# Kernel tuning notes

Hardware: AMD Instinct MI355X
Metric: run time of the kernel (lower is better)

## Reference

```python
import jax, jax.numpy as jnp
import numpy as np

B, C, H, W = 8, 512, 64, 64
K = 19       # num classes (Cityscapes)
CT = 256     # transform channels


def _proj(x, w, g, b):
    # 1x1 conv (no bias) + folded eval-mode BatchNorm (per-channel scale g, bias b) + ReLU
    # x: [B,Cin,H,W], w: [Cout,Cin]
    y = jnp.einsum('bchw,oc->bohw', x, w)
    return jax.nn.relu(y * g[None, :, None, None] + b[None, :, None, None])


def setup_inputs() -> dict:
    key = jax.random.key(0)
    ks = jax.random.split(key, 12)
    s = lambda i, shape: jax.random.normal(ks[i], shape, jnp.float32) * 0.05
    ones = lambda n: jnp.ones((n,), jnp.float32)
    zeros = lambda n: jnp.zeros((n,), jnp.float32)
    return {
        'x': jax.random.normal(ks[0], (B, C, H, W), jnp.float32),
        'preds': jax.random.normal(ks[1], (B, K, H, W), jnp.float32),
        'feats_il': jax.random.normal(ks[2], (B, C, H, W), jnp.float32),
        # query_project: two 1x1 conv+BN+ReLU blocks
        'q_w1': s(3, (CT, C)), 'q_g1': ones(CT), 'q_b1': zeros(CT),
        'q_w2': s(4, (CT, CT)), 'q_g2': ones(CT), 'q_b2': zeros(CT),
        # key_project: two 1x1 conv+BN+ReLU blocks
        'k_w1': s(5, (CT, C)), 'k_g1': ones(CT), 'k_b1': zeros(CT),
        'k_w2': s(6, (CT, CT)), 'k_g2': ones(CT), 'k_b2': zeros(CT),
        # value_project: one 1x1 conv+BN+ReLU (value_out_norm=True)
        'v_w': s(7, (CT, C)), 'v_g': ones(CT), 'v_b': zeros(CT),
        # out_project: one 1x1 conv+BN+ReLU
        'o_w': s(8, (C, CT)), 'o_g': ones(C), 'o_b': zeros(C),
    }


def reference(x, preds, feats_il, q_w1, q_g1, q_b1, q_w2, q_g2, q_b2,
              k_w1, k_g1, k_b1, k_w2, k_g2, k_b2, v_w, v_g, v_b, o_w, o_g, o_b):
    b, c, h, w = x.shape
    k = preds.shape[1]
    hw = h * w
    feats = x.reshape(b, c, hw).transpose(0, 2, 1)        # [B,HW,C]
    logits = preds.reshape(b, k, hw).transpose(0, 2, 1)   # [B,HW,K]
    argmax = jnp.argmax(logits, axis=-1)                  # [B,HW]
    onehot = jax.nn.one_hot(argmax, k, dtype=x.dtype)     # [B,HW,K]
    NEG = jnp.asarray(-1e9, x.dtype)
    masked = jnp.where(onehot > 0, logits, NEG)
    # per-class softmax over the pixels assigned to that class
    wgt = jax.nn.softmax(masked, axis=1)                  # [B,HW,K]
    cls_feat = jnp.einsum('bpk,bpc->bkc', wgt, feats)     # [B,K,C]
    # scatter class descriptor back to every pixel of that class
    feats_sl = jnp.take_along_axis(cls_feat, argmax[:, :, None], axis=1)  # [B,HW,C]
    feats_sl = feats_sl.transpose(0, 2, 1).reshape(b, c, h, w)
    # SelfAttentionBlock: query from inputs, key/value from feats_sl
    q = _proj(_proj(x, q_w1, q_g1, q_b1), q_w2, q_g2, q_b2)
    kk = _proj(_proj(feats_sl, k_w1, k_g1, k_b1), k_w2, k_g2, k_b2)
    v = _proj(feats_sl, v_w, v_g, v_b)
    ct = q.shape[1]
    qf = q.reshape(b, ct, hw).transpose(0, 2, 1)          # [B,HW,CT]
    kf = kk.reshape(b, ct, hw)                            # [B,CT,HW]
    vf = v.reshape(b, ct, hw).transpose(0, 2, 1)          # [B,HW,CT]
    sim = jnp.einsum('bqc,bck->bqk', qf, kf) * (ct ** -0.5)
    attn = jax.nn.softmax(sim, axis=-1)
    ctx = jnp.einsum('bqk,bkc->bqc', attn, vf)            # [B,HW,CT]
    ctx = ctx.transpose(0, 2, 1).reshape(b, ct, h, w)
    return _proj(ctx, o_w, o_g, o_b)
```

## Files before the change

kernel.cpp:

```cpp
#include <hip/hip_runtime.h>
#include <math.h>

#define HW 4096
#define NB 8
#define NK 19
#define CIN 512
#define CTC 256

typedef __attribute__((ext_vector_type(8))) short short8;
typedef __attribute__((ext_vector_type(4))) float f32x4;

__device__ inline unsigned short f2bf(float x) {
  unsigned u = __float_as_uint(x);
  return (unsigned short)((u + 0x7fffu + ((u >> 16) & 1u)) >> 16);
}
__device__ inline float bf2f(unsigned short h) {
  return __uint_as_float(((unsigned)h) << 16);
}
__device__ inline void gload16(const void* g, void* l) {
  __builtin_amdgcn_global_load_lds(
      (const __attribute__((address_space(1))) void*)g,
      (__attribute__((address_space(3))) void*)l, 16, 0, 0);
}

__global__ __launch_bounds__(256) void wk1a(
    const float* __restrict__ w1, const float* __restrict__ w2,
    const float* __restrict__ wo, unsigned short* __restrict__ wb1,
    unsigned short* __restrict__ wb2, unsigned short* __restrict__ wbo,
    uint4* __restrict__ cls_feat_z, const float* __restrict__ preds,
    float* __restrict__ bestg, int* __restrict__ clsg,
    unsigned int* __restrict__ Mu_part, unsigned int* __restrict__ cnt_part) {
  __shared__ unsigned int Mw[NK];
  __shared__ unsigned int Cw[NK];
  int bx = blockIdx.x;
  int tid = threadIdx.x;
  if (bx < 320) {
    int gid = bx * 256 + tid;
    int i = gid * 4;
    const float* src;
    unsigned short* dst;
    int off;
    if (i < 131072) { src = w1; dst = wb1; off = i; }
    else if (i < 196608) { src = w2; dst = wb2; off = i - 131072; }
    else { src = wo; dst = wbo; off = i - 196608; }
    float4 v = *(const float4*)(src + off);
    dst[off + 0] = f2bf(v.x);
    dst[off + 1] = f2bf(v.y);
    dst[off + 2] = f2bf(v.z);
    dst[off + 3] = f2bf(v.w);
    uint4 z = {0u, 0u, 0u, 0u};
    for (int j = gid; j < 19456; j += 81920) cls_feat_z[j] = z;
  } else {
    int bq = bx - 320;
    int b = bq >> 4, pblk = bq & 15;
    if (tid < NK) { Mw[tid] = 0u; Cw[tid] = 0u; }
    __syncthreads();
    int p = pblk * 256 + tid;
    const float* pb = preds + (size_t)b * NK * HW;
    float best = pb[p];
    int bi = 0;
#pragma unroll
    for (int k = 1; k < NK; ++k) {
      float v = pb[k * HW + p];
      if (v > best) { best = v; bi = k; }
    }
    bestg[b * HW + p] = best;
    clsg[b * HW + p] = bi;
    unsigned fb = __float_as_uint(best);
    unsigned key = (fb & 0x80000000u) ? ~fb : (fb | 0x80000000u);
    atomicMax(&Mw[bi], key);
    atomicAdd(&Cw[bi], 1u);
    __syncthreads();
    if (tid < 32) {
      Mu_part[(b * 16 + pblk) * 32 + tid] = (tid < NK) ? Mw[tid] : 0u;
      cnt_part[(b * 16 + pblk) * 32 + tid] = (tid < NK) ? Cw[tid] : 0u;
    }
  }
}

__global__ __launch_bounds__(256) void k1b(
    float* __restrict__ bestg, const int* __restrict__ clsg,
    const unsigned int* __restrict__ Mu_part, float* __restrict__ Zf_part) {
  int b = blockIdx.y, pblk = blockIdx.x;
  int tid = threadIdx.x;
  __shared__ float Mf[NK];
  __shared__ float Zw[NK];
  if (tid < NK) {
    unsigned key = 0u;
#pragma unroll
    for (int j = 0; j < 16; ++j) {
      unsigned v = Mu_part[(b * 16 + j) * 32 + tid];
      key = (v > key) ? v : key;
    }
    float m = -1e30f;
    if (key) {
      unsigned fb = (key & 0x80000000u) ? (key & 0x7fffffffu) : ~key;
      m = __uint_as_float(fb);
    }
    Mf[tid] = m;
    Zw[tid] = 0.f;
  }
  __syncthreads();
  int p = pblk * 256 + tid;
  int c = clsg[b * HW + p];
  float e = expf(bestg[b * HW + p] - Mf[c]);
  bestg[b * HW + p] = e;
  atomicAdd(&Zw[c], e);
  __syncthreads();
  if (tid < 32) Zf_part[(b * 16 + pblk) * 32 + tid] = (tid < NK) ? Zw[tid] : 0.f;
}

__global__ __launch_bounds__(256) void xk2(
    const float* __restrict__ x, const float* __restrict__ eg,
    const int* __restrict__ clsg, const float* __restrict__ Zf_part,
    unsigned short* __restrict__ xT, float* __restrict__ cls_feat) {
  __shared__ float tile[64][65];
  __shared__ unsigned short Bs[32 * 516];
  __shared__ float Zl[NK];
  int b = blockIdx.z, c0 = blockIdx.y * 64, pbase = blockIdx.x * 512;
  int tid = threadIdx.x;
  int l = tid & 63, w = tid >> 6;
  if (tid < NK) {
    float s = 0.f;
#pragma unroll
    for (int j = 0; j < 16; ++j) s += Zf_part[(b * 16 + j) * 32 + tid];
    Zl[tid] = s;
  }
  {
    uint4 z = {0u, 0u, 0u, 0u};
    for (int i = tid; i < 2064; i += 256) ((uint4*)Bs)[i] = z;
  }
  __syncthreads();
  for (int i = tid; i < 512; i += 256) {
    int c = clsg[b * HW + pbase + i];
    Bs[c * 516 + i] = f2bf(eg[b * HW + pbase + i] / Zl[c]);
  }
  f32x4 acc[2];
  acc[0] = (f32x4){0.f, 0.f, 0.f, 0.f};
  acc[1] = (f32x4){0.f, 0.f, 0.f, 0.f};
  int cbase = w * 16;
  for (int s = 0; s < 8; ++s) {
    int ps = pbase + s * 64;
    __syncthreads();
#pragma unroll
    for (int r = 0; r < 4; ++r) {
      int cl = r * 16 + (tid >> 4);
      int pl = (tid & 15) * 4;
      float4 v = *(const float4*)&x[((size_t)b * CIN + c0 + cl) * HW + ps + pl];
      tile[cl][pl + 0] = v.x;
      tile[cl][pl + 1] = v.y;
      tile[cl][pl + 2] = v.z;
      tile[cl][pl + 3] = v.w;
    }
    __syncthreads();
#pragma unroll
    for (int j = 0; j < 16; ++j) {
      int ploc = j * 4 + w;
      xT[((size_t)b * HW + ps + ploc) * CIN + c0 + l] = f2bf(tile[l][ploc]);
    }
#pragma unroll
    for (int ch = 0; ch < 2; ++ch) {
      int pt = ch * 32 + (l >> 4) * 8;
      union { short8 v; unsigned short u[8]; } af;
      const float* tp = &tile[cbase + (l & 15)][pt];
#pragma unroll
      for (int j = 0; j < 8; ++j) af.u[j] = f2bf(tp[j]);
      int pg = s * 64 + pt;
#pragma unroll
      for (int mf = 0; mf < 2; ++mf) {
        short8 bf = *(const short8*)&Bs[(mf * 16 + (l & 15)) * 516 + pg];
        acc[mf] =
            __builtin_amdgcn_mfma_f32_16x16x32_bf16(af.v, bf, acc[mf], 0, 0, 0);
      }
    }
  }
#pragma unroll
  for (int mf = 0; mf < 2; ++mf) {
    int k = mf * 16 + (l & 15);
    if (k < NK) {
#pragma unroll
      for (int r = 0; r < 4; ++r) {
        int c = c0 + cbase + (l >> 4) * 4 + r;
        atomicAdd(&cls_feat[((size_t)b * NK + k) * CIN + c], acc[mf][r]);
      }
    }
  }
}

__global__ __launch_bounds__(256) void k3a(
    const float* __restrict__ cls_feat, const float* __restrict__ kw1,
    const float* __restrict__ kg1, const float* __restrict__ kb1,
    const float* __restrict__ vw, const float* __restrict__ vg,
    const float* __restrict__ vb, float* __restrict__ h1g,
    float* __restrict__ Vcls) {
  int bk = blockIdx.y;
  int b = bk / NK, kc = bk % NK;
  int q = blockIdx.x;
  __shared__ float cf[CIN];
  int tid = threadIdx.x;
  const float* row = cls_feat + (size_t)bk * CIN;
  for (int i = tid; i < CIN; i += 256) cf[i] = row[i];
  __syncthreads();
  int o = tid >> 1, half = tid & 1;
  int col = q * 64 + (o & 63);
  const float* w =
      (o < 64) ? &kw1[(size_t)col * CIN] : &vw[(size_t)col * CIN];
  int base = half * 256;
  float acc[4] = {0.f, 0.f, 0.f, 0.f};
#pragma unroll 8
  for (int i = 0; i < 64; ++i) {
    float4 w4 = *(const float4*)&w[base + i * 4];
    const float* c4 = &cf[base + i * 4];
    acc[i & 3] += w4.x * c4[0] + w4.y * c4[1] + w4.z * c4[2] + w4.w * c4[3];
  }
  float s = (acc[0] + acc[1]) + (acc[2] + acc[3]);
  s += __shfl_xor(s, 1);
  if (half == 0) {
    if (o < 64) {
      h1g[(size_t)bk * CTC + col] = fmaxf(s * kg1[col] + kb1[col], 0.f);
    } else {
      Vcls[((size_t)b * CTC + col) * NK + kc] =
          fmaxf(s * vg[col] + vb[col], 0.f);
    }
  }
}

__global__ __launch_bounds__(256) void k3b(
    const float* __restrict__ h1g, const float* __restrict__ kw2,
    const float* __restrict__ kg2, const float* __restrict__ kb2,
    unsigned short* __restrict__ KclsT) {
  int bk = blockIdx.y;
  int q = blockIdx.x;
  __shared__ float h1[CTC];
  int tid = threadIdx.x;
  const float* row = h1g + (size_t)bk * CTC;
  if (tid < CTC) h1[tid] = row[tid];
  __syncthreads();
  int o = tid >> 2, part = tid & 3;
  int col = q * 64 + o;
  const float* w = &kw2[(size_t)col * CTC + part * 64];
  const float* c = &h1[part * 64];
  float acc[4] = {0.f, 0.f, 0.f, 0.f};
#pragma unroll
  for (int i = 0; i < 16; ++i) {
    float4 w4 = *(const float4*)&w[i * 4];
    acc[i & 3] += w4.x * c[i * 4] + w4.y * c[i * 4 + 1] + w4.z * c[i * 4 + 2] +
                  w4.w * c[i * 4 + 3];
  }
  float s = (acc[0] + acc[1]) + (acc[2] + acc[3]);
  s += __shfl_xor(s, 1);
  s += __shfl_xor(s, 2);
  if (part == 0)
    KclsT[(size_t)bk * CTC + col] = f2bf(fmaxf(s * kg2[col] + kb2[col], 0.f));
}

template <int KD>
__global__ __launch_bounds__(256) void gemm_mfma(
    const unsigned short* __restrict__ A, const unsigned short* __restrict__ Wb,
    const float* __restrict__ g, const float* __restrict__ bb,
    void* __restrict__ Y, int M, int outmode) {
  __shared__ __align__(16) unsigned short As[2][128 * 32];
  __shared__ __align__(16) unsigned short Bs[2][128 * 32];
  int b = blockIdx.z;
  int n0 = blockIdx.x * 128;
  int m0 = blockIdx.y * 128;
  int tid = threadIdx.x;
  int l = tid & 63, wid = tid >> 6;
  int wr = wid >> 1, wc = wid & 1;
  const unsigned short* Ab = A + (size_t)b * HW * KD;

  f32x4 acc[4][4];
#pragma unroll
  for (int i = 0; i < 4; ++i)
#pragma unroll
    for (int j = 0; j < 4; ++j) acc[i][j] = (f32x4){0.f, 0.f, 0.f, 0.f};

  const int NT = KD / 32;
  auto STAGE = [&](int buf, int t) {
    int k0 = t * 32;
#pragma unroll
    for (int q = 0; q < 2; ++q) {
      int e = q * 2048 + tid * 8;
      int rl = e >> 5, sl = (e >> 3) & 3;
      gload16(Ab + (size_t)(n0 + rl) * KD + k0 + 8 * (sl ^ ((rl >> 1) & 3)),
              &As[buf][q * 2048 + wid * 512]);
    }
#pragma unroll
    for (int q = 0; q < 2; ++q) {
      int e = q * 2048 + tid * 8;
      int rl = e >> 5, sl = (e >> 3) & 3;
      gload16(Wb + (size_t)(m0 + rl) * KD + k0 + 8 * (sl ^ ((rl >> 1) & 3)),
              &Bs[buf][q * 2048 + wid * 512]);
    }
  };
  STAGE(0, 0);
  for (int t = 0; t < NT; ++t) {
    __syncthreads();
    if (t + 1 < NT) STAGE((t + 1) & 1, t + 1);
    int cur = t & 1;
    short8 af[4], bf[4];
#pragma unroll
    for (int f = 0; f < 4; ++f) {
      int nl = wr * 64 + f * 16 + (l & 15);
      af[f] = *(const short8*)&As[cur][nl * 32 + 8 * ((l >> 4) ^ ((nl >> 1) & 3))];
      int ml = wc * 64 + f * 16 + (l & 15);
      bf[f] = *(const short8*)&Bs[cur][ml * 32 + 8 * ((l >> 4) ^ ((ml >> 1) & 3))];
    }
#pragma unroll
    for (int i = 0; i < 4; ++i)
#pragma unroll
      for (int j = 0; j < 4; ++j)
        acc[i][j] =
            __builtin_amdgcn_mfma_f32_16x16x32_bf16(af[i], bf[j], acc[i][j], 0, 0, 0);
  }
  if (outmode == 0) {
    float* Yf = (float*)Y + (size_t)b * M * HW;
#pragma unroll
    for (int j = 0; j < 4; ++j) {
      int m = m0 + wc * 64 + j * 16 + (l & 15);
      float gm = g[m], bm = bb[m];
#pragma unroll
      for (int i = 0; i < 4; ++i) {
        int n = n0 + wr * 64 + i * 16 + (l >> 4) * 4;
        float4 o;
        o.x = fmaxf(acc[i][j][0] * gm + bm, 0.f);
        o.y = fmaxf(acc[i][j][1] * gm + bm, 0.f);
        o.z = fmaxf(acc[i][j][2] * gm + bm, 0.f);
        o.w = fmaxf(acc[i][j][3] * gm + bm, 0.f);
        *(float4*)&Yf[(size_t)m * HW + n] = o;
      }
    }
  } else {
    unsigned short* Yt = (unsigned short*)Y + (size_t)b * HW * M;
#pragma unroll
    for (int j = 0; j < 4; ++j) {
      int m = m0 + wc * 64 + j * 16 + (l & 15);
      float gm = g[m], bm = bb[m];
#pragma unroll
      for (int i = 0; i < 4; ++i) {
        int n = n0 + wr * 64 + i * 16 + (l >> 4) * 4;
#pragma unroll
        for (int r = 0; r < 4; ++r)
          Yt[(size_t)(n + r) * M + m] = f2bf(fmaxf(acc[i][j][r] * gm + bm, 0.f));
      }
    }
  }
}

__global__ __launch_bounds__(256, 1) void g2k5(
    const unsigned short* __restrict__ q1T, const unsigned short* __restrict__ W2,
    const float* __restrict__ g2, const float* __restrict__ b2,
    const unsigned short* __restrict__ KclsT, const float* __restrict__ Vcls,
    const unsigned int* __restrict__ cnt_part, unsigned short* __restrict__ ctxT) {
  __shared__ __align__(16) char RC[49152];
  __shared__ __align__(16) unsigned short Qf[8][4096];
  __shared__ __align__(16) unsigned short Kl2[32 * 32 * 8];
  __shared__ __align__(16) unsigned short Vl2[4 * 256 * 8];
  __shared__ float cntl[NK];
  unsigned short* As = (unsigned short*)RC;
  unsigned short* Bs = (unsigned short*)(RC + 16384);
  float* simT = (float*)RC;
  unsigned short* Pl = (unsigned short*)(RC + 16896);

  int b = blockIdx.y;
  int p0 = blockIdx.x * 128;
  int tid = threadIdx.x;
  int l = tid & 63, w = tid >> 6;
  const unsigned short* q1b = q1T + ((size_t)b * HW + p0) * CTC;

  for (int i = tid; i < NK * 32; i += 256) {
    int m = i >> 5, s = i & 31;
    short8 v = *(const short8*)&KclsT[((size_t)b * NK + m) * CTC + s * 8];
    *(short8*)&Kl2[(s * 32 + m) * 8] = v;
  }
  for (int i = tid; i < 4 * 256; i += 256) {
    int s = i >> 8, c = i & 255;
    union { short8 v; unsigned short u[8]; } pk;
    const float* vr = &Vcls[((size_t)b * CTC + c) * NK];
#pragma unroll
    for (int j = 0; j < 8; ++j) {
      int k = s * 8 + j;
      pk.u[j] = (k < NK) ? f2bf(vr[k]) : (unsigned short)0;
    }
    *(short8*)&Vl2[(s * 256 + c) * 8] = pk.v;
  }
  if (tid < NK) {
    unsigned int s = 0u;
#pragma unroll
    for (int j = 0; j < 16; ++j) s += cnt_part[(b * 16 + j) * 32 + tid];
    cntl[tid] = (float)s;
  }

  auto STAGE_A = [&](int buf, int t) {
    int k0 = t * 32;
#pragma unroll
    for (int q = 0; q < 2; ++q) {
      int e = q * 2048 + tid * 8;
      int rl = e >> 5, sl = (e >> 3) & 3;
      gload16(q1b + (size_t)rl * CTC + k0 + 8 * (sl ^ ((rl >> 1) & 3)),
              &As[buf * 4096 + q * 2048 + w * 512]);
    }
  };
  auto STAGE_B = [&](int buf, int t) {
    int k0 = t * 32;
#pragma unroll
    for (int q = 0; q < 4; ++q) {
      int e = q * 2048 + tid * 8;
      int rl = e >> 5, sl = (e >> 3) & 3;
      gload16(W2 + (size_t)rl * CTC + k0 + 8 * (sl ^ ((rl >> 1) & 3)),
              &Bs[buf * 8192 + q * 2048 + w * 512]);
    }
  };
  f32x4 acc[2][16];
#pragma unroll
  for (int i = 0; i < 2; ++i)
#pragma unroll
    for (int j = 0; j < 16; ++j) acc[i][j] = (f32x4){0.f, 0.f, 0.f, 0.f};
  STAGE_A(0, 0);
  STAGE_B(0, 0);
  for (int t = 0; t < 8; ++t) {
    __syncthreads();
    if (t + 1 < 8) { STAGE_A((t + 1) & 1, t + 1); STAGE_B((t + 1) & 1, t + 1); }
    int cur = t & 1;
    short8 af[2];
#pragma unroll
    for (int f = 0; f < 2; ++f) {
      int nl = w * 32 + f * 16 + (l & 15);
      af[f] =
          *(const short8*)&As[cur * 4096 + nl * 32 + 8 * ((l >> 4) ^ ((nl >> 1) & 3))];
    }
#pragma unroll
    for (int mf = 0; mf < 16; ++mf) {
      int ml = mf * 16 + (l & 15);
      short8 bf =
          *(const short8*)&Bs[cur * 8192 + ml * 32 + 8 * ((l >> 4) ^ ((ml >> 1) & 3))];
      acc[0][mf] =
          __builtin_amdgcn_mfma_f32_16x16x32_bf16(af[0], bf, acc[0][mf], 0, 0, 0);
      acc[1][mf] =
          __builtin_amdgcn_mfma_f32_16x16x32_bf16(af[1], bf, acc[1][mf], 0, 0, 0);
    }
  }
#pragma unroll
  for (int mf = 0; mf < 16; ++mf) {
    int ch = mf * 16 + (l & 15);
    float gm = g2[ch], bm = b2[ch];
    int tq = ch >> 5, slot = (ch >> 3) & 3, wi = ch & 7;
#pragma unroll
    for (int i = 0; i < 2; ++i) {
#pragma unroll
      for (int r = 0; r < 4; ++r) {
        int p = w * 32 + i * 16 + (l >> 4) * 4 + r;
        Qf[tq][p * 32 + 8 * (slot ^ ((p >> 1) & 3)) + wi] =
            f2bf(fmaxf(acc[i][mf][r] * gm + bm, 0.f));
      }
    }
  }
  __syncthreads();

  f32x4 a2[2][2];
#pragma unroll
  for (int i = 0; i < 2; ++i)
#pragma unroll
    for (int j = 0; j < 2; ++j) a2[i][j] = (f32x4){0.f, 0.f, 0.f, 0.f};
  for (int t = 0; t < 8; ++t) {
    short8 aq[2], bk[2];
#pragma unroll
    for (int f = 0; f < 2; ++f) {
      int nl = w * 32 + f * 16 + (l & 15);
      aq[f] = *(const short8*)&Qf[t][nl * 32 + 8 * ((l >> 4) ^ ((nl >> 1) & 3))];
      int s = t * 4 + (l >> 4);
      int ml = f * 16 + (l & 15);
      bk[f] = *(const short8*)&Kl2[(s * 32 + ml) * 8];
    }
#pragma unroll
    for (int i = 0; i < 2; ++i)
#pragma unroll
      for (int j = 0; j < 2; ++j)
        a2[i][j] =
            __builtin_amdgcn_mfma_f32_16x16x32_bf16(aq[i], bk[j], a2[i][j], 0, 0, 0);
  }
  __syncthreads();
#pragma unroll
  for (int i = 0; i < 2; ++i)
#pragma unroll
    for (int j = 0; j < 2; ++j) {
      int m = j * 16 + (l & 15);
      if (m < NK) {
#pragma unroll
        for (int r = 0; r < 4; ++r) {
          int p = w * 32 + i * 16 + (l >> 4) * 4 + r;
          simT[p * 33 + m] = a2[i][j][r];
        }
      }
    }
  __syncthreads();
  if (tid < 128) {
    float sims[NK];
#pragma unroll
    for (int k = 0; k < NK; ++k) sims[k] = simT[tid * 33 + k] * 0.0625f;
    float m = -1e30f;
#pragma unroll
    for (int k = 0; k < NK; ++k)
      if (cntl[k] > 0.f) m = fmaxf(m, sims[k]);
    float d = 0.f;
#pragma unroll
    for (int k = 0; k < NK; ++k) {
      float e = (cntl[k] > 0.f) ? expf(sims[k] - m) : 0.f;
      sims[k] = cntl[k] * e;
      d += sims[k];
    }
    float inv = 1.f / d;
#pragma unroll
    for (int s = 0; s < 4; ++s) {
      union { short8 v; unsigned short u8[8]; } pk;
#pragma unroll
      for (int j = 0; j < 8; ++j) {
        int k = s * 8 + j;
        pk.u8[j] = (k < NK) ? f2bf(sims[k] * inv) : (unsigned short)0;
      }
      *(short8*)&Pl[(s * 128 + tid) * 8] = pk.v;
    }
  }
  __syncthreads();
  short8 ap[2];
#pragma unroll
  for (int f = 0; f < 2; ++f) {
    int nl = w * 32 + f * 16 + (l & 15);
    ap[f] = *(const short8*)&Pl[((l >> 4) * 128 + nl) * 8];
  }
  unsigned short* cb = ctxT + ((size_t)b * HW + p0) * CTC;
#pragma unroll
  for (int mc = 0; mc < 4; ++mc) {
#pragma unroll
    for (int mf = 0; mf < 4; ++mf) {
      int ml = mc * 64 + mf * 16 + (l & 15);
      short8 bv = *(const short8*)&Vl2[((l >> 4) * 256 + ml) * 8];
#pragma unroll
      for (int nf = 0; nf < 2; ++nf) {
        f32x4 z = {0.f, 0.f, 0.f, 0.f};
        f32x4 o = __builtin_amdgcn_mfma_f32_16x16x32_bf16(ap[nf], bv, z, 0, 0, 0);
#pragma unroll
        for (int r = 0; r < 4; ++r) {
          int p = w * 32 + nf * 16 + (l >> 4) * 4 + r;
          cb[(size_t)p * CTC + ml] = f2bf(o[r]);
        }
      }
    }
  }
}

extern "C" void kernel_launch(void* const* d_in, const int* in_sizes, int n_in,
                              void* d_out, int out_size, void* d_ws, size_t ws_size,
                              hipStream_t stream) {
  const float* x = (const float*)d_in[0];
  const float* preds = (const float*)d_in[1];
  const float* q_w1 = (const float*)d_in[3];
  const float* q_g1 = (const float*)d_in[4];
  const float* q_b1 = (const float*)d_in[5];
  const float* q_w2 = (const float*)d_in[6];
  const float* q_g2 = (const float*)d_in[7];
  const float* q_b2 = (const float*)d_in[8];
  const float* k_w1 = (const float*)d_in[9];
  const float* k_g1 = (const float*)d_in[10];
  const float* k_b1 = (const float*)d_in[11];
  const float* k_w2 = (const float*)d_in[12];
  const float* k_g2 = (const float*)d_in[13];
  const float* k_b2 = (const float*)d_in[14];
  const float* v_w = (const float*)d_in[15];
  const float* v_g = (const float*)d_in[16];
  const float* v_b = (const float*)d_in[17];
  const float* o_w = (const float*)d_in[18];
  const float* o_g = (const float*)d_in[19];
  const float* o_b = (const float*)d_in[20];
  float* out = (float*)d_out;

  char* base = (char*)d_ws;
  unsigned short* xT = (unsigned short*)base;
  unsigned short* q1T = (unsigned short*)(base + 33554432);
  unsigned short* ctxT = q1T;
  char* f32r = base + 50331648;
  float* cls_feat = (float*)f32r;
  unsigned short* KclsT = (unsigned short*)(f32r + 311296);
  float* Vcls = (float*)(f32r + 389120);
  unsigned short* wb1 = (unsigned short*)(f32r + 544768);
  unsigned short* wb2 = (unsigned short*)(f32r + 806912);
  unsigned short* wbo = (unsigned short*)(f32r + 937984);
  float* h1g = (float*)(f32r + 1200128);
  float* bestg = (float*)(f32r + 1355776);
  int* clsg = (int*)(f32r + 1486848);
  unsigned int* Mu_part = (unsigned int*)(f32r + 1617920);
  unsigned int* cnt_part = (unsigned int*)(f32r + 1634304);
  float* Zf_part = (float*)(f32r + 1650688);

  wk1a<<<448, 256, 0, stream>>>(q_w1, q_w2, o_w, wb1, wb2, wbo,
                                (uint4*)cls_feat, preds, bestg, clsg, Mu_part,
                                cnt_part);
  k1b<<<dim3(16, NB), 256, 0, stream>>>(bestg, clsg, Mu_part, Zf_part);
  xk2<<<dim3(8, 8, NB), 256, 0, stream>>>(x, bestg, clsg, Zf_part, xT,
                                          cls_feat);
  k3a<<<dim3(4, NB * NK), 256, 0, stream>>>(cls_feat, k_w1, k_g1, k_b1, v_w,
                                            v_g, v_b, h1g, Vcls);
  k3b<<<dim3(4, NB * NK), 256, 0, stream>>>(h1g, k_w2, k_g2, k_b2, KclsT);
  gemm_mfma<CIN><<<dim3(32, 2, NB), 256, 0, stream>>>(xT, wb1, q_g1, q_b1,
                                                      (void*)q1T, CTC, 1);
  g2k5<<<dim3(HW / 128, NB), 256, 0, stream>>>(q1T, wb2, q_g2, q_b2, KclsT,
                                               Vcls, cnt_part, ctxT);
  gemm_mfma<CTC><<<dim3(32, 4, NB), 256, 0, stream>>>(ctxT, wbo, o_g, o_b,
                                                      (void*)out, CIN, 0);
}
```

Measured before the change: 127.4 us.

## Fuse first query projection GEMM into attention kernel via LDS intermediate

```diff
diff --git a/kernel.cpp b/kernel.cpp
--- a/kernel.cpp
+++ b/kernel.cpp
@@ -347,13 +347,15 @@
   }
 }
 
-__global__ __launch_bounds__(256, 1) void g2k5(
-    const unsigned short* __restrict__ q1T, const unsigned short* __restrict__ W2,
-    const float* __restrict__ g2, const float* __restrict__ b2,
-    const unsigned short* __restrict__ KclsT, const float* __restrict__ Vcls,
-    const unsigned int* __restrict__ cnt_part, unsigned short* __restrict__ ctxT) {
+__global__ __launch_bounds__(256, 1) void g1g2k5(
+    const unsigned short* __restrict__ xT, const unsigned short* __restrict__ W1,
+    const float* __restrict__ g1, const float* __restrict__ b1,
+    const unsigned short* __restrict__ W2, const float* __restrict__ g2,
+    const float* __restrict__ b2, const unsigned short* __restrict__ KclsT,
+    const float* __restrict__ Vcls, const unsigned int* __restrict__ cnt_part,
+    unsigned short* __restrict__ ctxT) {
   __shared__ __align__(16) char RC[49152];
-  __shared__ __align__(16) unsigned short Qf[8][4096];
+  __shared__ __align__(16) unsigned short Q1f[8][4096];
   __shared__ __align__(16) unsigned short Kl2[32 * 32 * 8];
   __shared__ __align__(16) unsigned short Vl2[4 * 256 * 8];
   __shared__ float cntl[NK];
@@ -366,7 +368,7 @@
   int p0 = blockIdx.x * 128;
   int tid = threadIdx.x;
   int l = tid & 63, w = tid >> 6;
-  const unsigned short* q1b = q1T + ((size_t)b * HW + p0) * CTC;
+  const unsigned short* xTb = xT + ((size_t)b * HW + p0) * CIN;
 
   for (int i = tid; i < NK * 32; i += 256) {
     int m = i >> 5, s = i & 31;
@@ -391,36 +393,37 @@
     cntl[tid] = (float)s;
   }
 
-  auto STAGE_A = [&](int buf, int t) {
+  f32x4 acc[2][16];
+
+  auto STAGE_A1 = [&](int buf, int t) {
     int k0 = t * 32;
 #pragma unroll
     for (int q = 0; q < 2; ++q) {
       int e = q * 2048 + tid * 8;
       int rl = e >> 5, sl = (e >> 3) & 3;
-      gload16(q1b + (size_t)rl * CTC + k0 + 8 * (sl ^ ((rl >> 1) & 3)),
+      gload16(xTb + (size_t)rl * CIN + k0 + 8 * (sl ^ ((rl >> 1) & 3)),
               &As[buf * 4096 + q * 2048 + w * 512]);
     }
   };
-  auto STAGE_B = [&](int buf, int t) {
+  auto STAGE_B1 = [&](int buf, int t) {
     int k0 = t * 32;
 #pragma unroll
     for (int q = 0; q < 4; ++q) {
       int e = q * 2048 + tid * 8;
       int rl = e >> 5, sl = (e >> 3) & 3;
-      gload16(W2 + (size_t)rl * CTC + k0 + 8 * (sl ^ ((rl >> 1) & 3)),
+      gload16(W1 + (size_t)rl * CIN + k0 + 8 * (sl ^ ((rl >> 1) & 3)),
               &Bs[buf * 8192 + q * 2048 + w * 512]);
     }
   };
-  f32x4 acc[2][16];
 #pragma unroll
   for (int i = 0; i < 2; ++i)
 #pragma unroll
     for (int j = 0; j < 16; ++j) acc[i][j] = (f32x4){0.f, 0.f, 0.f, 0.f};
-  STAGE_A(0, 0);
-  STAGE_B(0, 0);
-  for (int t = 0; t < 8; ++t) {
+  STAGE_A1(0, 0);
+  STAGE_B1(0, 0);
+  for (int t = 0; t < 16; ++t) {
     __syncthreads();
-    if (t + 1 < 8) { STAGE_A((t + 1) & 1, t + 1); STAGE_B((t + 1) & 1, t + 1); }
+    if (t + 1 < 16) { STAGE_A1((t + 1) & 1, t + 1); STAGE_B1((t + 1) & 1, t + 1); }
     int cur = t & 1;
     short8 af[2];
 #pragma unroll
@@ -443,6 +446,59 @@
 #pragma unroll
   for (int mf = 0; mf < 16; ++mf) {
     int ch = mf * 16 + (l & 15);
+    float gm = g1[ch], bm = b1[ch];
+    int tq = ch >> 5, slot = (ch >> 3) & 3, wi = ch & 7;
+#pragma unroll
+    for (int i = 0; i < 2; ++i) {
+#pragma unroll
+      for (int r = 0; r < 4; ++r) {
+        int p = w * 32 + i * 16 + (l >> 4) * 4 + r;
+        Q1f[tq][p * 32 + 8 * (slot ^ ((p >> 1) & 3)) + wi] =
+            f2bf(fmaxf(acc[i][mf][r] * gm + bm, 0.f));
+      }
+    }
+  }
+
+  auto STAGE_B2 = [&](int buf, int t) {
+    int k0 = t * 32;
+#pragma unroll
+    for (int q = 0; q < 4; ++q) {
+      int e = q * 2048 + tid * 8;
+      int rl = e >> 5, sl = (e >> 3) & 3;
+      gload16(W2 + (size_t)rl * CTC + k0 + 8 * (sl ^ ((rl >> 1) & 3)),
+              &Bs[buf * 8192 + q * 2048 + w * 512]);
+    }
+  };
+#pragma unroll
+  for (int i = 0; i < 2; ++i)
+#pragma unroll
+    for (int j = 0; j < 16; ++j) acc[i][j] = (f32x4){0.f, 0.f, 0.f, 0.f};
+  STAGE_B2(0, 0);
+  for (int t = 0; t < 8; ++t) {
+    __syncthreads();
+    if (t + 1 < 8) STAGE_B2((t + 1) & 1, t + 1);
+    int cur = t & 1;
+    short8 af[2];
+#pragma unroll
+    for (int f = 0; f < 2; ++f) {
+      int nl = w * 32 + f * 16 + (l & 15);
+      af[f] = *(const short8*)&Q1f[t][nl * 32 + 8 * ((l >> 4) ^ ((nl >> 1) & 3))];
+    }
+#pragma unroll
+    for (int mf = 0; mf < 16; ++mf) {
+      int ml = mf * 16 + (l & 15);
+      short8 bf =
+          *(const short8*)&Bs[cur * 8192 + ml * 32 + 8 * ((l >> 4) ^ ((ml >> 1) & 3))];
+      acc[0][mf] =
+          __builtin_amdgcn_mfma_f32_16x16x32_bf16(af[0], bf, acc[0][mf], 0, 0, 0);
+      acc[1][mf] =
+          __builtin_amdgcn_mfma_f32_16x16x32_bf16(af[1], bf, acc[1][mf], 0, 0, 0);
+    }
+  }
+  __syncthreads();
+#pragma unroll
+  for (int mf = 0; mf < 16; ++mf) {
+    int ch = mf * 16 + (l & 15);
     float gm = g2[ch], bm = b2[ch];
     int tq = ch >> 5, slot = (ch >> 3) & 3, wi = ch & 7;
 #pragma unroll
@@ -450,7 +506,7 @@
 #pragma unroll
       for (int r = 0; r < 4; ++r) {
         int p = w * 32 + i * 16 + (l >> 4) * 4 + r;
-        Qf[tq][p * 32 + 8 * (slot ^ ((p >> 1) & 3)) + wi] =
+        Q1f[tq][p * 32 + 8 * (slot ^ ((p >> 1) & 3)) + wi] =
             f2bf(fmaxf(acc[i][mf][r] * gm + bm, 0.f));
       }
     }
@@ -467,7 +523,7 @@
 #pragma unroll
     for (int f = 0; f < 2; ++f) {
       int nl = w * 32 + f * 16 + (l & 15);
-      aq[f] = *(const short8*)&Qf[t][nl * 32 + 8 * ((l >> 4) ^ ((nl >> 1) & 3))];
+      aq[f] = *(const short8*)&Q1f[t][nl * 32 + 8 * ((l >> 4) ^ ((nl >> 1) & 3))];
       int s = t * 4 + (l >> 4);
       int ml = f * 16 + (l & 15);
       bk[f] = *(const short8*)&Kl2[(s * 32 + ml) * 8];
@@ -576,8 +632,7 @@
 
   char* base = (char*)d_ws;
   unsigned short* xT = (unsigned short*)base;
-  unsigned short* q1T = (unsigned short*)(base + 33554432);
-  unsigned short* ctxT = q1T;
+  unsigned short* ctxT = (unsigned short*)(base + 33554432);
   char* f32r = base + 50331648;
   float* cls_feat = (float*)f32r;
   unsigned short* KclsT = (unsigned short*)(f32r + 311296);
@@ -601,10 +656,9 @@
   k3a<<<dim3(4, NB * NK), 256, 0, stream>>>(cls_feat, k_w1, k_g1, k_b1, v_w,
                                             v_g, v_b, h1g, Vcls);
   k3b<<<dim3(4, NB * NK), 256, 0, stream>>>(h1g, k_w2, k_g2, k_b2, KclsT);
-  gemm_mfma<CIN><<<dim3(32, 2, NB), 256, 0, stream>>>(xT, wb1, q_g1, q_b1,
-                                                      (void*)q1T, CTC, 1);
-  g2k5<<<dim3(HW / 128, NB), 256, 0, stream>>>(q1T, wb2, q_g2, q_b2, KclsT,
-                                               Vcls, cnt_part, ctxT);
+  g1g2k5<<<dim3(HW / 128, NB), 256, 0, stream>>>(xT, wb1, q_g1, q_b1, wb2,
+                                                 q_g2, q_b2, KclsT, Vcls,
+                                                 cnt_part, ctxT);
   gemm_mfma<CTC><<<dim3(32, 4, NB), 256, 0, stream>>>(ctxT, wbo, o_g, o_b,
                                                       (void*)out, CIN, 0);
 }
```

Result: no change. 128.8 us (+1.1%).
